# Kernel optimization log

Hardware: AMD Instinct MI355X
Metric: run time of the kernel (lower is better)

Reference implementation:

```python
import jax, jax.numpy as jnp
import numpy as np

D_MODEL = 2048
N_HEADS = 16
D_HEAD = 128
ROPE_BASE = 10000.0


def setup_inputs() -> dict:
    key = jax.random.key(0)
    ks = jax.random.split(key, 5)
    s = 0.02
    x = jax.random.normal(ks[0], (2, 4096, D_MODEL), dtype=jnp.float32)
    Wq = jax.random.normal(ks[1], (N_HEADS * D_HEAD, D_MODEL), dtype=jnp.float32) * s
    Wk = jax.random.normal(ks[2], (N_HEADS * D_HEAD, D_MODEL), dtype=jnp.float32) * s
    Wv = jax.random.normal(ks[3], (N_HEADS * D_HEAD, D_MODEL), dtype=jnp.float32) * s
    Wo = jax.random.normal(ks[4], (D_MODEL, N_HEADS * D_HEAD), dtype=jnp.float32) * s
    return {"x": x, "Wq": Wq, "Wk": Wk, "Wv": Wv, "Wo": Wo}


def _rope_tables(seq_len, dtype):
    inv_freq = 1.0 / (ROPE_BASE ** (jnp.arange(0, D_HEAD, 2, dtype=jnp.float32) / D_HEAD))
    freqs = jnp.arange(seq_len, dtype=jnp.float32)[:, None] * inv_freq[None, :]  # (S, D/2)
    cos = jnp.repeat(jnp.cos(freqs), 2, axis=-1).astype(dtype)  # (S, D)
    sin = jnp.repeat(jnp.sin(freqs), 2, axis=-1).astype(dtype)
    return cos, sin


def _rotate_half(x):
    # interleaved pairs: (x0,x1,...) -> (-x1,x0,-x3,x2,...)
    x1 = x[..., ::2]
    x2 = x[..., 1::2]
    return jnp.stack([-x2, x1], axis=-1).reshape(x.shape)


def reference(x, Wq, Wk, Wv, Wo):
    B, S, _ = x.shape
    H, D = N_HEADS, D_HEAD
    q = jnp.einsum('bsd,ed->bse', x, Wq).reshape(B, S, H, D).transpose(0, 2, 1, 3)
    k = jnp.einsum('bsd,ed->bse', x, Wk).reshape(B, S, H, D).transpose(0, 2, 1, 3)
    v = jnp.einsum('bsd,ed->bse', x, Wv).reshape(B, S, H, D).transpose(0, 2, 1, 3)
    cos, sin = _rope_tables(S, x.dtype)  # (S, D)
    q = q * cos + _rotate_half(q) * sin
    k = k * cos + _rotate_half(k) * sin
    # causal scaled dot-product attention
    scale = 1.0 / jnp.sqrt(jnp.asarray(D, dtype=x.dtype))
    scores = jnp.einsum('bhqd,bhkd->bhqk', q, k) * scale
    mask = jnp.tril(jnp.ones((S, S), dtype=bool))
    scores = jnp.where(mask, scores, jnp.finfo(x.dtype).min)
    probs = jax.nn.softmax(scores, axis=-1)
    a = jnp.einsum('bhqk,bhkd->bhqd', probs, v)
    a = a.transpose(0, 2, 1, 3).reshape(B, S, H * D)
    return jnp.einsum('bse,de->bsd', a, Wo)
```

## Files before the change

### kernel.cpp

```cpp
#include <hip/hip_runtime.h>

typedef float f32x4 __attribute__((ext_vector_type(4)));
typedef short bf16x8 __attribute__((ext_vector_type(8)));

#define DEVI __device__ __forceinline__

constexpr int Bn = 2;
constexpr int Sn = 4096;
constexpr int Hn = 16;
constexpr int Dn = 128;
constexpr int En = 2048;
constexpr int Mtot = Bn * Sn;

DEVI unsigned short f2bf(float f) {
  unsigned u = __float_as_uint(f);
  u += 0x7fffu + ((u >> 16) & 1u);
  return (unsigned short)(u >> 16);
}
DEVI float bf2f(unsigned short h) {
  return __uint_as_float(((unsigned)h) << 16);
}

DEVI void async16(const void* g, void* l) {
  __builtin_amdgcn_global_load_lds(
      (const __attribute__((address_space(1))) void*)g,
      (__attribute__((address_space(3))) void*)l, 16, 0, 0);
}

__global__ void cvt_kernel(const float* __restrict__ in, ushort* __restrict__ out) {
  size_t i = ((size_t)blockIdx.x * 256 + threadIdx.x) * 4;
  float4 v = *(const float4*)&in[i];
  ushort4 o;
  o.x = f2bf(v.x); o.y = f2bf(v.y); o.z = f2bf(v.z); o.w = f2bf(v.w);
  *(ushort4*)&out[i] = o;
}

__global__ void rope_kernel(ushort* __restrict__ Q, float scale) {
  int row = blockIdx.x;
  int s = row & (Sn - 1);
  int t = threadIdx.x;
  size_t base = (size_t)row * En;
#pragma unroll
  for (int rep = 0; rep < 4; ++rep) {
    int p = rep * 256 + t;
    int e = p * 2;
    int pp = (e & (Dn - 1)) >> 1;
    float inv = exp2f(-(float)pp * (13.287712379549449f / 64.0f));
    float ang = (float)s * inv;
    float c = cosf(ang), sn = sinf(ang);
    unsigned v = *(unsigned*)&Q[base + e];
    float q0 = bf2f((unsigned short)(v & 0xffffu));
    float q1 = bf2f((unsigned short)(v >> 16));
    float n0 = (q0 * c - q1 * sn) * scale;
    float n1 = (q1 * c + q0 * sn) * scale;
    unsigned outv = (unsigned)f2bf(n0) | ((unsigned)f2bf(n1) << 16);
    *(unsigned*)&Q[base + e] = outv;
  }
}

template <int EPI>
__global__ __launch_bounds__(256) void gemm_bt(const ushort* __restrict__ A,
                                               const ushort* __restrict__ Bm,
                                               void* __restrict__ Cv) {
  __shared__ ushort As[128 * 64];
  __shared__ ushort Bs[128 * 64];
  const int t = threadIdx.x;
  const int lane = t & 63, w = t >> 6;
  const int ln = lane & 15, gq = lane >> 4;
  const int m0 = blockIdx.y * 128, n0 = blockIdx.x * 128;
  const int rm = (w >> 1) * 64, rn = (w & 1) * 64;
  f32x4 acc[4][4] = {};

  for (int k0 = 0; k0 < En; k0 += 64) {
#pragma unroll
    for (int rep = 0; rep < 4; ++rep) {
      int c = rep * 256 + t;
      int row = c >> 3, c8 = c & 7;
      async16(&A[(size_t)(m0 + row) * En + k0 + c8 * 8],
              (char*)As + (rep * 256 + w * 64) * 16);
      async16(&Bm[(size_t)(n0 + row) * En + k0 + c8 * 8],
              (char*)Bs + (rep * 256 + w * 64) * 16);
    }
    __syncthreads();
#pragma unroll
    for (int kk = 0; kk < 64; kk += 32) {
      bf16x8 af[4], bf[4];
#pragma unroll
      for (int i = 0; i < 4; ++i)
        af[i] = *(const bf16x8*)&As[(rm + i * 16 + ln) * 64 + kk + gq * 8];
#pragma unroll
      for (int j = 0; j < 4; ++j)
        bf[j] = *(const bf16x8*)&Bs[(rn + j * 16 + ln) * 64 + kk + gq * 8];
#pragma unroll
      for (int i = 0; i < 4; ++i)
#pragma unroll
        for (int j = 0; j < 4; ++j)
          acc[i][j] = __builtin_amdgcn_mfma_f32_16x16x32_bf16(af[i], bf[j], acc[i][j], 0, 0, 0);
    }
    __syncthreads();
  }

  if constexpr (EPI == 0) {
    ushort* C = (ushort*)Cv;
#pragma unroll
    for (int i = 0; i < 4; ++i) {
      int row0 = m0 + rm + i * 16 + gq * 4;
#pragma unroll
      for (int j = 0; j < 4; ++j) {
        int col = n0 + rn + j * 16 + ln;
#pragma unroll
        for (int r = 0; r < 4; ++r)
          C[(size_t)(row0 + r) * En + col] = f2bf(acc[i][j][r]);
      }
    }
  } else if constexpr (EPI == 1) {
    ushort* Vt = (ushort*)Cv;
#pragma unroll
    for (int i = 0; i < 4; ++i) {
      int mrow = m0 + rm + i * 16 + gq * 4;
      int bb = mrow >> 12;
      int ss = mrow & (Sn - 1);
#pragma unroll
      for (int j = 0; j < 4; ++j) {
        int col = n0 + rn + j * 16 + ln;
        ushort4 pk;
        pk.x = f2bf(acc[i][j][0]); pk.y = f2bf(acc[i][j][1]);
        pk.z = f2bf(acc[i][j][2]); pk.w = f2bf(acc[i][j][3]);
        *(ushort4*)&Vt[((size_t)(bb * En + col)) * Sn + ss] = pk;
      }
    }
  } else {
    float* C = (float*)Cv;
#pragma unroll
    for (int i = 0; i < 4; ++i) {
      int row0 = m0 + rm + i * 16 + gq * 4;
#pragma unroll
      for (int j = 0; j < 4; ++j) {
        int col = n0 + rn + j * 16 + ln;
#pragma unroll
        for (int r = 0; r < 4; ++r)
          C[(size_t)(row0 + r) * En + col] = acc[i][j][r];
      }
    }
  }
}

__global__ __launch_bounds__(256) void flash_kernel(const ushort* __restrict__ Qb,
                                                    const ushort* __restrict__ Kb,
                                                    const ushort* __restrict__ Vt,
                                                    ushort* __restrict__ Ab) {
  __shared__ ushort Ks[64 * 128];
  __shared__ ushort Vs[128 * 64];
  __shared__ ushort Ps[4][32 * 72];
  const int t = threadIdx.x;
  const int lane = t & 63, w = t >> 6;
  const int ln = lane & 15, gq = lane >> 4;
  const int swz = (ln & 7) << 3;
  const int q0 = (gridDim.y - 1 - blockIdx.y) * 128;
  const int bh = blockIdx.x;
  const int b = bh >> 4, h = bh & 15;

  bf16x8 qf[2][4];
#pragma unroll
  for (int it = 0; it < 2; ++it) {
    int qrow = q0 + w * 32 + it * 16 + ln;
    size_t base = ((size_t)(b * Sn + qrow)) * En + h * Dn;
#pragma unroll
    for (int ks = 0; ks < 4; ++ks)
      qf[it][ks] = *(const bf16x8*)&Qb[base + ks * 32 + gq * 8];
  }

  f32x4 o[8][2] = {};
  float m_prev[2] = {-1e30f, -1e30f};
  float l_prev[2] = {0.f, 0.f};

  for (int j0 = 0; j0 <= q0 + 64; j0 += 64) {
#pragma unroll
    for (int rep = 0; rep < 4; ++rep) {
      int c = rep * 256 + t;
      int krow = c >> 4, kcs = c & 15;
      int kc = kcs ^ (krow & 7);
      async16(&Kb[((size_t)(b * Sn + j0 + krow)) * En + h * Dn + kc * 8],
              (char*)Ks + (rep * 256 + w * 64) * 16);
      int vrow = c >> 3, vcs = c & 7;
      int vc = vcs ^ (vrow & 7);
      async16(&Vt[((size_t)(b * En + h * Dn + vrow)) * Sn + j0 + vc * 8],
              (char*)Vs + (rep * 256 + w * 64) * 16);
    }
    __syncthreads();

    if (j0 <= q0 + w * 32 + 31) {
      f32x4 s[2][4] = {};
      __builtin_amdgcn_s_setprio(1);
#pragma unroll
      for (int jt = 0; jt < 4; ++jt) {
#pragma unroll
        for (int ks = 0; ks < 4; ++ks) {
          bf16x8 kf = *(const bf16x8*)&Ks[(((jt * 16 + ln) * 128 + ks * 32 + gq * 8)) ^ swz];
          s[0][jt] = __builtin_amdgcn_mfma_f32_16x16x32_bf16(kf, qf[0][ks], s[0][jt], 0, 0, 0);
          s[1][jt] = __builtin_amdgcn_mfma_f32_16x16x32_bf16(kf, qf[1][ks], s[1][jt], 0, 0, 0);
        }
      }
      __builtin_amdgcn_s_setprio(0);

#pragma unroll
      for (int it = 0; it < 2; ++it) {
        const int qbase = q0 + w * 32 + it * 16;
        const int qrow = qbase + ln;
        float mx = -1e30f;
        if (j0 + 63 > qbase) {
#pragma unroll
          for (int jt = 0; jt < 4; ++jt)
#pragma unroll
            for (int r = 0; r < 4; ++r) {
              int j = j0 + jt * 16 + gq * 4 + r;
              float v = s[it][jt][r];
              if (j > qrow) v = -1e30f;
              s[it][jt][r] = v;
              mx = fmaxf(mx, v);
            }
        } else {
#pragma unroll
          for (int jt = 0; jt < 4; ++jt)
#pragma unroll
            for (int r = 0; r < 4; ++r)
              mx = fmaxf(mx, s[it][jt][r]);
        }
        mx = fmaxf(mx, __shfl_xor(mx, 16));
        mx = fmaxf(mx, __shfl_xor(mx, 32));
        float mn;
        if (__all(mx - m_prev[it] <= 8.f)) {
          mn = m_prev[it];
        } else {
          mn = fmaxf(m_prev[it], mx);
          float alpha = exp2f(m_prev[it] - mn);
          m_prev[it] = mn;
          l_prev[it] *= alpha;
#pragma unroll
          for (int dt = 0; dt < 8; ++dt) o[dt][it] *= alpha;
        }
        float sum = 0.f;
#pragma unroll
        for (int jt = 0; jt < 4; ++jt) {
#pragma unroll
          for (int r = 0; r < 4; ++r) {
            float p = exp2f(s[it][jt][r] - mn);
            s[it][jt][r] = p;
            sum += p;
          }
        }
        sum += __shfl_xor(sum, 16);
        sum += __shfl_xor(sum, 32);
        l_prev[it] += sum;
#pragma unroll
        for (int jt = 0; jt < 4; ++jt) {
          ushort4 pk;
          pk.x = f2bf(s[it][jt][0]); pk.y = f2bf(s[it][jt][1]);
          pk.z = f2bf(s[it][jt][2]); pk.w = f2bf(s[it][jt][3]);
          *(ushort4*)&Ps[w][(it * 16 + ln) * 72 + jt * 16 + gq * 4] = pk;
        }
      }

      __builtin_amdgcn_s_setprio(1);
#pragma unroll
      for (int ksj = 0; ksj < 2; ++ksj) {
        bf16x8 pf[2];
#pragma unroll
        for (int it = 0; it < 2; ++it)
          pf[it] = *(const bf16x8*)&Ps[w][(it * 16 + ln) * 72 + ksj * 32 + gq * 8];
#pragma unroll
        for (int dt = 0; dt < 8; ++dt) {
          bf16x8 vf = *(const bf16x8*)&Vs[(((dt * 16 + ln) * 64 + ksj * 32 + gq * 8)) ^ swz];
          o[dt][0] = __builtin_amdgcn_mfma_f32_16x16x32_bf16(vf, pf[0], o[dt][0], 0, 0, 0);
          o[dt][1] = __builtin_amdgcn_mfma_f32_16x16x32_bf16(vf, pf[1], o[dt][1], 0, 0, 0);
        }
      }
      __builtin_amdgcn_s_setprio(0);
    }
    __syncthreads();
  }

#pragma unroll
  for (int it = 0; it < 2; ++it) {
    float inv = 1.f / l_prev[it];
    int qrow = q0 + w * 32 + it * 16 + ln;
    size_t base = ((size_t)(b * Sn + qrow)) * En + h * Dn;
#pragma unroll
    for (int dt = 0; dt < 8; ++dt) {
      ushort4 pk;
      pk.x = f2bf(o[dt][it][0] * inv);
      pk.y = f2bf(o[dt][it][1] * inv);
      pk.z = f2bf(o[dt][it][2] * inv);
      pk.w = f2bf(o[dt][it][3] * inv);
      *(ushort4*)&Ab[base + dt * 16 + gq * 4] = pk;
    }
  }
}

extern "C" void kernel_launch(void* const* d_in, const int* in_sizes, int n_in,
                              void* d_out, int out_size, void* d_ws, size_t ws_size,
                              hipStream_t stream) {
  const float* x  = (const float*)d_in[0];
  const float* Wq = (const float*)d_in[1];
  const float* Wk = (const float*)d_in[2];
  const float* Wv = (const float*)d_in[3];
  const float* Wo = (const float*)d_in[4];

  char* ws = (char*)d_ws;
  ushort* xb  = (ushort*)(ws + 0);
  ushort* wqb = (ushort*)(ws + 33554432);
  ushort* wkb = (ushort*)(ws + 41943040);
  ushort* wvb = (ushort*)(ws + 50331648);
  ushort* wob = (ushort*)(ws + 58720256);
  ushort* Qb  = (ushort*)(ws + 67108864);
  ushort* Kb  = (ushort*)(ws + 100663296);
  ushort* Vt  = (ushort*)(ws + 134217728);
  ushort* Ab  = xb;

  cvt_kernel<<<dim3(Mtot * En / 1024), 256, 0, stream>>>(x, xb);
  cvt_kernel<<<dim3(En * En / 1024), 256, 0, stream>>>(Wq, wqb);
  cvt_kernel<<<dim3(En * En / 1024), 256, 0, stream>>>(Wk, wkb);
  cvt_kernel<<<dim3(En * En / 1024), 256, 0, stream>>>(Wv, wvb);
  cvt_kernel<<<dim3(En * En / 1024), 256, 0, stream>>>(Wo, wob);

  dim3 ggrid(En / 128, Mtot / 128);
  gemm_bt<0><<<ggrid, 256, 0, stream>>>(xb, wqb, (void*)Qb);
  gemm_bt<0><<<ggrid, 256, 0, stream>>>(xb, wkb, (void*)Kb);
  gemm_bt<1><<<ggrid, 256, 0, stream>>>(xb, wvb, (void*)Vt);

  rope_kernel<<<dim3(Mtot), 256, 0, stream>>>(Qb, 0.08838834764831845f * 1.4426950408889634f);
  rope_kernel<<<dim3(Mtot), 256, 0, stream>>>(Kb, 1.0f);

  flash_kernel<<<dim3(Bn * Hn, Sn / 128), 256, 0, stream>>>(Qb, Kb, Vt, Ab);

  gemm_bt<2><<<ggrid, 256, 0, stream>>>(Ab, wob, d_out);
}
```

Baseline: 922.7 us.

## Double-buffer K/V tiles in flash attention and remap blocks for XCD locality

The flash kernel now prefetches the next K/V tile into a second LDS buffer while computing on the current one, using explicit vmcnt waits and barriers in place of a load-then-sync loop. The P scratch buffer drops its padding and uses an XOR swizzle. Both the flash kernel and the GEMM remap block IDs so that blocks sharing a head or a weight tile land on the same XCD, which is meant to improve L2 reuse. Doubling the K/V LDS footprint may lower occupancy, and the hand-written vmcnt counts must match the number of async loads issued.

```diff
diff --git a/kernel.cpp b/kernel.cpp
--- a/kernel.cpp
+++ b/kernel.cpp
@@ -67,7 +67,9 @@
   const int t = threadIdx.x;
   const int lane = t & 63, w = t >> 6;
   const int ln = lane & 15, gq = lane >> 4;
-  const int m0 = blockIdx.y * 128, n0 = blockIdx.x * 128;
+  const int orig = blockIdx.y * 16 + blockIdx.x;
+  const int lid = (orig & 7) * 128 + (orig >> 3);
+  const int m0 = (lid >> 4) * 128, n0 = (lid & 15) * 128;
   const int rm = (w >> 1) * 64, rn = (w & 1) * 64;
   f32x4 acc[4][4] = {};
 
@@ -149,15 +151,19 @@
                                                     const ushort* __restrict__ Kb,
                                                     const ushort* __restrict__ Vt,
                                                     ushort* __restrict__ Ab) {
-  __shared__ ushort Ks[64 * 128];
-  __shared__ ushort Vs[128 * 64];
-  __shared__ ushort Ps[4][32 * 72];
+  __shared__ ushort Ks[2][64 * 128];
+  __shared__ ushort Vs[2][128 * 64];
+  __shared__ ushort Ps[4][32 * 64];
   const int t = threadIdx.x;
   const int lane = t & 63, w = t >> 6;
   const int ln = lane & 15, gq = lane >> 4;
   const int swz = (ln & 7) << 3;
-  const int q0 = (gridDim.y - 1 - blockIdx.y) * 128;
-  const int bh = blockIdx.x;
+
+  const int orig = blockIdx.x;
+  const int pos = orig >> 3;
+  const int bh = ((orig & 7) << 2) + (pos >> 5);
+  const int qt = 31 - (pos & 31);
+  const int q0 = qt * 128;
   const int b = bh >> 4, h = bh & 15;
 
   bf16x8 qf[2][4];
@@ -174,20 +180,37 @@
   float m_prev[2] = {-1e30f, -1e30f};
   float l_prev[2] = {0.f, 0.f};
 
-  for (int j0 = 0; j0 <= q0 + 64; j0 += 64) {
+  const int last = 2 * qt + 1;
+
+  auto stage = [&](int jt0, int bufi) {
 #pragma unroll
     for (int rep = 0; rep < 4; ++rep) {
       int c = rep * 256 + t;
       int krow = c >> 4, kcs = c & 15;
       int kc = kcs ^ (krow & 7);
-      async16(&Kb[((size_t)(b * Sn + j0 + krow)) * En + h * Dn + kc * 8],
-              (char*)Ks + (rep * 256 + w * 64) * 16);
+      async16(&Kb[((size_t)(b * Sn + jt0 + krow)) * En + h * Dn + kc * 8],
+              (char*)&Ks[bufi][0] + (rep * 256 + w * 64) * 16);
       int vrow = c >> 3, vcs = c & 7;
       int vc = vcs ^ (vrow & 7);
-      async16(&Vt[((size_t)(b * En + h * Dn + vrow)) * Sn + j0 + vc * 8],
-              (char*)Vs + (rep * 256 + w * 64) * 16);
-    }
-    __syncthreads();
+      async16(&Vt[((size_t)(b * En + h * Dn + vrow)) * Sn + jt0 + vc * 8],
+              (char*)&Vs[bufi][0] + (rep * 256 + w * 64) * 16);
+    }
+  };
+
+  stage(0, 0);
+
+  for (int tt = 0; tt <= last; ++tt) {
+    const int cur = tt & 1;
+    const int j0 = tt << 6;
+    __builtin_amdgcn_s_barrier();
+    if (tt < last) {
+      stage((tt + 1) << 6, cur ^ 1);
+      asm volatile("s_waitcnt vmcnt(8)" ::: "memory");
+    } else {
+      asm volatile("s_waitcnt vmcnt(0)" ::: "memory");
+    }
+    __builtin_amdgcn_s_barrier();
+    __builtin_amdgcn_sched_barrier(0);
 
     if (j0 <= q0 + w * 32 + 31) {
       f32x4 s[2][4] = {};
@@ -196,7 +219,7 @@
       for (int jt = 0; jt < 4; ++jt) {
 #pragma unroll
         for (int ks = 0; ks < 4; ++ks) {
-          bf16x8 kf = *(const bf16x8*)&Ks[(((jt * 16 + ln) * 128 + ks * 32 + gq * 8)) ^ swz];
+          bf16x8 kf = *(const bf16x8*)&Ks[cur][(((jt * 16 + ln) * 128 + ks * 32 + gq * 8)) ^ swz];
           s[0][jt] = __builtin_amdgcn_mfma_f32_16x16x32_bf16(kf, qf[0][ks], s[0][jt], 0, 0, 0);
           s[1][jt] = __builtin_amdgcn_mfma_f32_16x16x32_bf16(kf, qf[1][ks], s[1][jt], 0, 0, 0);
         }
@@ -257,7 +280,7 @@
           ushort4 pk;
           pk.x = f2bf(s[it][jt][0]); pk.y = f2bf(s[it][jt][1]);
           pk.z = f2bf(s[it][jt][2]); pk.w = f2bf(s[it][jt][3]);
-          *(ushort4*)&Ps[w][(it * 16 + ln) * 72 + jt * 16 + gq * 4] = pk;
+          *(ushort4*)&Ps[w][((it * 16 + ln) * 64 + jt * 16 + gq * 4) ^ swz] = pk;
         }
       }
 
@@ -267,17 +290,16 @@
         bf16x8 pf[2];
 #pragma unroll
         for (int it = 0; it < 2; ++it)
-          pf[it] = *(const bf16x8*)&Ps[w][(it * 16 + ln) * 72 + ksj * 32 + gq * 8];
+          pf[it] = *(const bf16x8*)&Ps[w][((it * 16 + ln) * 64 + ksj * 32 + gq * 8) ^ swz];
 #pragma unroll
         for (int dt = 0; dt < 8; ++dt) {
-          bf16x8 vf = *(const bf16x8*)&Vs[(((dt * 16 + ln) * 64 + ksj * 32 + gq * 8)) ^ swz];
+          bf16x8 vf = *(const bf16x8*)&Vs[cur][(((dt * 16 + ln) * 64 + ksj * 32 + gq * 8)) ^ swz];
           o[dt][0] = __builtin_amdgcn_mfma_f32_16x16x32_bf16(vf, pf[0], o[dt][0], 0, 0, 0);
           o[dt][1] = __builtin_amdgcn_mfma_f32_16x16x32_bf16(vf, pf[1], o[dt][1], 0, 0, 0);
         }
       }
       __builtin_amdgcn_s_setprio(0);
     }
-    __syncthreads();
   }
 
 #pragma unroll
@@ -331,7 +353,7 @@
   rope_kernel<<<dim3(Mtot), 256, 0, stream>>>(Qb, 0.08838834764831845f * 1.4426950408889634f);
   rope_kernel<<<dim3(Mtot), 256, 0, stream>>>(Kb, 1.0f);
 
-  flash_kernel<<<dim3(Bn * Hn, Sn / 128), 256, 0, stream>>>(Qb, Kb, Vt, Ab);
+  flash_kernel<<<dim3(Bn * Hn * Sn / 128), 256, 0, stream>>>(Qb, Kb, Vt, Ab);
 
   gemm_bt<2><<<ggrid, 256, 0, stream>>>(Ab, wob, d_out);
 }
```

New measurement: 959.9 us. +4.0%, slower.

## Rewrite flash attention with 32x32 MFMA and register-resident P

Applied to the files above, without the earlier changes.

Moves the flash attention kernel from 16x16x32 MFMA tiles to 32x32x16 MFMA, so each wave handles 32 query rows as one tile. The softmax probabilities are packed to bf16 in registers and exchanged across half-waves with shuffles instead of going through the Ps shared-memory buffer. The grid is flattened to 1D with a remapped block-to-(batch, head, query-tile) order for scheduling across CUs, and the K swizzle pattern changes to match the new load layout. The aim is fewer LDS round trips and MFMA instructions per tile. In exchange it adds cross-lane shuffles and higher register pressure.

```diff
diff --git a/kernel.cpp b/kernel.cpp
--- a/kernel.cpp
+++ b/kernel.cpp
@@ -1,6 +1,7 @@
 #include <hip/hip_runtime.h>
 
 typedef float f32x4 __attribute__((ext_vector_type(4)));
+typedef float f32x16 __attribute__((ext_vector_type(16)));
 typedef short bf16x8 __attribute__((ext_vector_type(8)));
 
 #define DEVI __device__ __forceinline__
@@ -20,11 +21,28 @@
 DEVI float bf2f(unsigned short h) {
   return __uint_as_float(((unsigned)h) << 16);
 }
+DEVI unsigned pk2(float a, float b) {
+  return (unsigned)f2bf(a) | ((unsigned)f2bf(b) << 16);
+}
 
 DEVI void async16(const void* g, void* l) {
   __builtin_amdgcn_global_load_lds(
       (const __attribute__((address_space(1))) void*)g,
       (__attribute__((address_space(3))) void*)l, 16, 0, 0);
+}
+
+DEVI bf16x8 pack_pa(float a0, float a1, float a2, float a3,
+                    float a4, float a5, float a6, float a7, int hi) {
+  unsigned w0 = pk2(a0, a1), w1 = pk2(a2, a3);
+  unsigned y0 = pk2(a4, a5), y1 = pk2(a6, a7);
+  unsigned x0 = __shfl_xor(w0, 32), x1 = __shfl_xor(w1, 32);
+  unsigned z0 = __shfl_xor(y0, 32), z1 = __shfl_xor(y1, 32);
+  union { unsigned u[4]; bf16x8 v; } r;
+  r.u[0] = hi ? z0 : w0;
+  r.u[1] = hi ? z1 : w1;
+  r.u[2] = hi ? y0 : x0;
+  r.u[3] = hi ? y1 : x1;
+  return r.v;
 }
 
 __global__ void cvt_kernel(const float* __restrict__ in, ushort* __restrict__ out) {
@@ -151,148 +169,132 @@
                                                     ushort* __restrict__ Ab) {
   __shared__ ushort Ks[64 * 128];
   __shared__ ushort Vs[128 * 64];
-  __shared__ ushort Ps[4][32 * 72];
   const int t = threadIdx.x;
   const int lane = t & 63, w = t >> 6;
-  const int ln = lane & 15, gq = lane >> 4;
-  const int swz = (ln & 7) << 3;
-  const int q0 = (gridDim.y - 1 - blockIdx.y) * 128;
-  const int bh = blockIdx.x;
+  const int l31 = lane & 31, hi = lane >> 5;
+
+  const int orig = blockIdx.x;
+  const int pos = orig >> 3;
+  const int bh = ((orig & 7) << 2) + (pos >> 5);
+  const int qt = 31 - (pos & 31);
+  const int q0 = qt * 128;
   const int b = bh >> 4, h = bh & 15;
 
-  bf16x8 qf[2][4];
-#pragma unroll
-  for (int it = 0; it < 2; ++it) {
-    int qrow = q0 + w * 32 + it * 16 + ln;
-    size_t base = ((size_t)(b * Sn + qrow)) * En + h * Dn;
-#pragma unroll
-    for (int ks = 0; ks < 4; ++ks)
-      qf[it][ks] = *(const bf16x8*)&Qb[base + ks * 32 + gq * 8];
-  }
-
-  f32x4 o[8][2] = {};
-  float m_prev[2] = {-1e30f, -1e30f};
-  float l_prev[2] = {0.f, 0.f};
-
-  for (int j0 = 0; j0 <= q0 + 64; j0 += 64) {
+  const int qrow = q0 + w * 32 + l31;
+
+  bf16x8 qf[8];
+  {
+    size_t qbase = ((size_t)(b * Sn + qrow)) * En + h * Dn + hi * 8;
+#pragma unroll
+    for (int ks = 0; ks < 8; ++ks)
+      qf[ks] = *(const bf16x8*)&Qb[qbase + ks * 16];
+  }
+
+  f32x16 o[4] = {};
+  float m_prev = -1e30f, l_prev = 0.f;
+  const int last = 2 * qt + 1;
+
+  for (int tt = 0; tt <= last; ++tt) {
+    const int j0 = tt << 6;
 #pragma unroll
     for (int rep = 0; rep < 4; ++rep) {
       int c = rep * 256 + t;
-      int krow = c >> 4, kcs = c & 15;
-      int kc = kcs ^ (krow & 7);
+      int krow = c >> 4, ksl = c & 15;
+      int kc = ksl ^ (krow & 15);
       async16(&Kb[((size_t)(b * Sn + j0 + krow)) * En + h * Dn + kc * 8],
               (char*)Ks + (rep * 256 + w * 64) * 16);
-      int vrow = c >> 3, vcs = c & 7;
-      int vc = vcs ^ (vrow & 7);
+      int vrow = c >> 3, vsl = c & 7;
+      int vc = vsl ^ (vrow & 7);
       async16(&Vt[((size_t)(b * En + h * Dn + vrow)) * Sn + j0 + vc * 8],
               (char*)Vs + (rep * 256 + w * 64) * 16);
     }
     __syncthreads();
 
     if (j0 <= q0 + w * 32 + 31) {
-      f32x4 s[2][4] = {};
+      f32x16 s0 = {}, s1 = {};
       __builtin_amdgcn_s_setprio(1);
 #pragma unroll
-      for (int jt = 0; jt < 4; ++jt) {
+      for (int ks = 0; ks < 8; ++ks) {
+        int soff = ((ks * 2 + hi) ^ (l31 & 15)) << 3;
+        bf16x8 kf0 = *(const bf16x8*)&Ks[l31 * 128 + soff];
+        bf16x8 kf1 = *(const bf16x8*)&Ks[(32 + l31) * 128 + soff];
+        s0 = __builtin_amdgcn_mfma_f32_32x32x16_bf16(kf0, qf[ks], s0, 0, 0, 0);
+        s1 = __builtin_amdgcn_mfma_f32_32x32x16_bf16(kf1, qf[ks], s1, 0, 0, 0);
+      }
+      __builtin_amdgcn_s_setprio(0);
+
+      float mx = -1e30f;
+      if (j0 + 63 > q0 + w * 32) {
+#pragma unroll
+        for (int r = 0; r < 16; ++r) {
+          int jj = j0 + (r & 3) + 8 * (r >> 2) + 4 * hi;
+          if (jj > qrow) s0[r] = -1e30f;
+          if (jj + 32 > qrow) s1[r] = -1e30f;
+          mx = fmaxf(mx, fmaxf(s0[r], s1[r]));
+        }
+      } else {
+#pragma unroll
+        for (int r = 0; r < 16; ++r)
+          mx = fmaxf(mx, fmaxf(s0[r], s1[r]));
+      }
+      mx = fmaxf(mx, __shfl_xor(mx, 32));
+
+      float mn;
+      if (__all(mx - m_prev <= 8.f)) {
+        mn = m_prev;
+      } else {
+        mn = fmaxf(m_prev, mx);
+        float alpha = exp2f(m_prev - mn);
+        m_prev = mn;
+        l_prev *= alpha;
+#pragma unroll
+        for (int d = 0; d < 4; ++d) o[d] *= alpha;
+      }
+      float sum = 0.f;
+#pragma unroll
+      for (int r = 0; r < 16; ++r) {
+        float p0 = exp2f(s0[r] - mn);
+        float p1 = exp2f(s1[r] - mn);
+        s0[r] = p0; s1[r] = p1;
+        sum += p0 + p1;
+      }
+      sum += __shfl_xor(sum, 32);
+      l_prev += sum;
+
+      bf16x8 pa[4];
+      pa[0] = pack_pa(s0[0], s0[1], s0[2], s0[3], s0[4], s0[5], s0[6], s0[7], hi);
+      pa[1] = pack_pa(s0[8], s0[9], s0[10], s0[11], s0[12], s0[13], s0[14], s0[15], hi);
+      pa[2] = pack_pa(s1[0], s1[1], s1[2], s1[3], s1[4], s1[5], s1[6], s1[7], hi);
+      pa[3] = pack_pa(s1[8], s1[9], s1[10], s1[11], s1[12], s1[13], s1[14], s1[15], hi);
+
+      __builtin_amdgcn_s_setprio(1);
+#pragma unroll
+      for (int dsub = 0; dsub < 4; ++dsub) {
+        int d = dsub * 32 + l31;
 #pragma unroll
         for (int ks = 0; ks < 4; ++ks) {
-          bf16x8 kf = *(const bf16x8*)&Ks[(((jt * 16 + ln) * 128 + ks * 32 + gq * 8)) ^ swz];
-          s[0][jt] = __builtin_amdgcn_mfma_f32_16x16x32_bf16(kf, qf[0][ks], s[0][jt], 0, 0, 0);
-          s[1][jt] = __builtin_amdgcn_mfma_f32_16x16x32_bf16(kf, qf[1][ks], s[1][jt], 0, 0, 0);
+          int soff = ((ks * 2 + hi) ^ (d & 7)) << 3;
+          bf16x8 vf = *(const bf16x8*)&Vs[d * 64 + soff];
+          o[dsub] = __builtin_amdgcn_mfma_f32_32x32x16_bf16(vf, pa[ks], o[dsub], 0, 0, 0);
         }
       }
       __builtin_amdgcn_s_setprio(0);
-
-#pragma unroll
-      for (int it = 0; it < 2; ++it) {
-        const int qbase = q0 + w * 32 + it * 16;
-        const int qrow = qbase + ln;
-        float mx = -1e30f;
-        if (j0 + 63 > qbase) {
-#pragma unroll
-          for (int jt = 0; jt < 4; ++jt)
-#pragma unroll
-            for (int r = 0; r < 4; ++r) {
-              int j = j0 + jt * 16 + gq * 4 + r;
-              float v = s[it][jt][r];
-              if (j > qrow) v = -1e30f;
-              s[it][jt][r] = v;
-              mx = fmaxf(mx, v);
-            }
-        } else {
-#pragma unroll
-          for (int jt = 0; jt < 4; ++jt)
-#pragma unroll
-            for (int r = 0; r < 4; ++r)
-              mx = fmaxf(mx, s[it][jt][r]);
-        }
-        mx = fmaxf(mx, __shfl_xor(mx, 16));
-        mx = fmaxf(mx, __shfl_xor(mx, 32));
-        float mn;
-        if (__all(mx - m_prev[it] <= 8.f)) {
-          mn = m_prev[it];
-        } else {
-          mn = fmaxf(m_prev[it], mx);
-          float alpha = exp2f(m_prev[it] - mn);
-          m_prev[it] = mn;
-          l_prev[it] *= alpha;
-#pragma unroll
-          for (int dt = 0; dt < 8; ++dt) o[dt][it] *= alpha;
-        }
-        float sum = 0.f;
-#pragma unroll
-        for (int jt = 0; jt < 4; ++jt) {
-#pragma unroll
-          for (int r = 0; r < 4; ++r) {
-            float p = exp2f(s[it][jt][r] - mn);
-            s[it][jt][r] = p;
-            sum += p;
-          }
-        }
-        sum += __shfl_xor(sum, 16);
-        sum += __shfl_xor(sum, 32);
-        l_prev[it] += sum;
-#pragma unroll
-        for (int jt = 0; jt < 4; ++jt) {
-          ushort4 pk;
-          pk.x = f2bf(s[it][jt][0]); pk.y = f2bf(s[it][jt][1]);
-          pk.z = f2bf(s[it][jt][2]); pk.w = f2bf(s[it][jt][3]);
-          *(ushort4*)&Ps[w][(it * 16 + ln) * 72 + jt * 16 + gq * 4] = pk;
-        }
-      }
-
-      __builtin_amdgcn_s_setprio(1);
-#pragma unroll
-      for (int ksj = 0; ksj < 2; ++ksj) {
-        bf16x8 pf[2];
-#pragma unroll
-        for (int it = 0; it < 2; ++it)
-          pf[it] = *(const bf16x8*)&Ps[w][(it * 16 + ln) * 72 + ksj * 32 + gq * 8];
-#pragma unroll
-        for (int dt = 0; dt < 8; ++dt) {
-          bf16x8 vf = *(const bf16x8*)&Vs[(((dt * 16 + ln) * 64 + ksj * 32 + gq * 8)) ^ swz];
-          o[dt][0] = __builtin_amdgcn_mfma_f32_16x16x32_bf16(vf, pf[0], o[dt][0], 0, 0, 0);
-          o[dt][1] = __builtin_amdgcn_mfma_f32_16x16x32_bf16(vf, pf[1], o[dt][1], 0, 0, 0);
-        }
-      }
-      __builtin_amdgcn_s_setprio(0);
     }
     __syncthreads();
   }
 
-#pragma unroll
-  for (int it = 0; it < 2; ++it) {
-    float inv = 1.f / l_prev[it];
-    int qrow = q0 + w * 32 + it * 16 + ln;
-    size_t base = ((size_t)(b * Sn + qrow)) * En + h * Dn;
-#pragma unroll
-    for (int dt = 0; dt < 8; ++dt) {
+  float inv = 1.f / l_prev;
+  size_t base = ((size_t)(b * Sn + qrow)) * En + h * Dn;
+#pragma unroll
+  for (int dsub = 0; dsub < 4; ++dsub) {
+#pragma unroll
+    for (int g = 0; g < 4; ++g) {
       ushort4 pk;
-      pk.x = f2bf(o[dt][it][0] * inv);
-      pk.y = f2bf(o[dt][it][1] * inv);
-      pk.z = f2bf(o[dt][it][2] * inv);
-      pk.w = f2bf(o[dt][it][3] * inv);
-      *(ushort4*)&Ab[base + dt * 16 + gq * 4] = pk;
+      pk.x = f2bf(o[dsub][g * 4 + 0] * inv);
+      pk.y = f2bf(o[dsub][g * 4 + 1] * inv);
+      pk.z = f2bf(o[dsub][g * 4 + 2] * inv);
+      pk.w = f2bf(o[dsub][g * 4 + 3] * inv);
+      *(ushort4*)&Ab[base + dsub * 32 + g * 8 + hi * 4] = pk;
     }
   }
 }
@@ -331,7 +333,7 @@
   rope_kernel<<<dim3(Mtot), 256, 0, stream>>>(Qb, 0.08838834764831845f * 1.4426950408889634f);
   rope_kernel<<<dim3(Mtot), 256, 0, stream>>>(Kb, 1.0f);
 
-  flash_kernel<<<dim3(Bn * Hn, Sn / 128), 256, 0, stream>>>(Qb, Kb, Vt, Ab);
+  flash_kernel<<<dim3(Bn * Hn * Sn / 128), 256, 0, stream>>>(Qb, Kb, Vt, Ab);
 
   gemm_bt<2><<<ggrid, 256, 0, stream>>>(Ab, wob, d_out);
 }
```

Measured after the change: 943.5 us. 1.02x slower.
